# Kernel optimization log

Hardware: AMD Instinct MI355X
Metric: run time of the kernel (lower is better)

## Reference

```python
import jax, jax.numpy as jnp
import numpy as np

SLOPE = 0.2

def setup_inputs() -> dict:
    key = jax.random.key(0)
    ks = jax.random.split(key, 24)
    B, O, M, Nb = 16, 1024, 64, 64
    in_ope, in_mas, in_arc, out = 16, 8, 8, 32
    f = lambda k, s: jax.random.normal(k, s, dtype=jnp.float32)
    adj = lambda k, s: jax.random.randint(k, s, 0, 2).astype(jnp.float32)
    return {
        'adj0': adj(ks[0], (O, M)),
        'adj1': adj(ks[1], (O, M)),
        'adj2': adj(ks[2], (O, Nb)),
        'adj3': adj(ks[3], (O, Nb)),
        'batch_idxes': jnp.arange(B, dtype=jnp.int64),
        'feat_opes': f(ks[4], (B, O, in_ope)),
        'feat_mas': f(ks[5], (B, M, in_mas)),
        'feat_buf': f(ks[6], (B, Nb, in_mas)),
        'feat_arc_ma_in': f(ks[7], (B, O, M, in_arc)),
        'feat_arc_buf_in': f(ks[8], (B, O, Nb, in_arc)),
        'feat_arc_ma_out': f(ks[9], (B, O, M, in_arc)),
        'feat_arc_buf_out': f(ks[10], (B, O, Nb, in_arc)),
        'W_ope': f(ks[11], (in_ope, out)) * 0.2,
        'W_mas': f(ks[12], (in_mas, out)) * 0.2,
        'W_buf': f(ks[13], (in_mas, out)) * 0.2,
        'W_arc_in': f(ks[14], (in_arc, out)) * 0.2,
        'W_arc_out': f(ks[15], (in_arc, out)) * 0.2,
        'attn_ope': jax.random.uniform(ks[16], (out,), dtype=jnp.float32),
        'attn_mas': jax.random.uniform(ks[17], (out,), dtype=jnp.float32),
        'attn_arc': jax.random.uniform(ks[18], (out,), dtype=jnp.float32),
    }

def _branch(adj_in, adj_out, p_ope, p_node, p_arc_in, p_arc_out, e_ope, e_node, e_arc_in, e_arc_out):
    # adj_*: [O,N]; e_ope: [B,O,1]; e_node: [B,N,1]; e_arc_*: [B,O,N,1]
    def scores(A2, e_arc):
        A = A2[None, :, :, None]                               # [1,O,N,1]
        a = A * e_ope[:, :, None, :] + e_arc + A * e_node[:, None, :, :]
        return jax.nn.leaky_relu(a, SLOPE)                     # [B,O,N,1]
    eik_in = scores(adj_in, e_arc_in)
    eik_out = scores(adj_out, e_arc_out)
    ekk = jax.nn.leaky_relu(e_node + e_node, SLOPE)            # [B,N,1]
    def alphas(A2, eik):
        e = jnp.concatenate([eik, ekk[:, None]], axis=1)       # [B,O+1,N,1]
        mask = jnp.concatenate([A2 == 1.0, jnp.ones((1, A2.shape[1]), dtype=bool)], axis=0)
        e = jnp.where(mask[None, :, :, None], e, -jnp.inf)
        return jax.nn.softmax(e[..., 0], axis=1)               # [B,O+1,N] over neighbors
    al_in = alphas(adj_in, eik_in)
    al_out = alphas(adj_out, eik_out)
    # NOTE: Wmu_out replicates the original's missing-parens expression exactly
    Wmu_in = jnp.sum((p_arc_in + p_ope[:, :, None, :]) * al_in[:, :-1, :, None], axis=1)   # [B,N,F]
    Wmu_out = jnp.sum(p_arc_out + p_ope[:, :, None, :] * al_out[:, :-1, :, None], axis=1)  # [B,N,F]
    Wmu_kk = p_node * (al_in[:, -1, :] + al_out[:, -1, :])[..., None]                      # [B,N,F]
    return jax.nn.sigmoid(Wmu_in + Wmu_out + Wmu_kk)

def reference(adj0, adj1, adj2, adj3, batch_idxes, feat_opes, feat_mas, feat_buf,
              feat_arc_ma_in, feat_arc_buf_in, feat_arc_ma_out, feat_arc_buf_out,
              W_ope, W_mas, W_buf, W_arc_in, W_arc_out, attn_ope, attn_mas, attn_arc):
    p_ope = feat_opes @ W_ope              # [B,O,F]
    p_mas = feat_mas @ W_mas               # [B,M,F]
    p_buf = feat_buf @ W_buf               # [B,Nb,F]
    p_arc_ma_in = feat_arc_ma_in @ W_arc_in
    p_arc_buf_in = feat_arc_buf_in @ W_arc_in
    p_arc_ma_out = feat_arc_ma_out @ W_arc_out
    p_arc_buf_out = feat_arc_buf_out @ W_arc_out
    score = lambda p, a: jnp.sum(p * a, axis=-1, keepdims=True)
    e_ope = score(p_ope, attn_ope)
    e_mas = score(p_mas, attn_mas)
    e_buf = score(p_buf, attn_mas)         # original uses attn_mas for buffers too
    nu_mas = _branch(adj0, adj1, p_ope, p_mas, p_arc_ma_in, p_arc_ma_out,
                     e_ope, e_mas, score(p_arc_ma_in, attn_arc), score(p_arc_ma_out, attn_arc))
    nu_buf = _branch(adj2, adj3, p_ope, p_buf, p_arc_buf_in, p_arc_buf_out,
                     e_ope, e_buf, score(p_arc_buf_in, attn_arc), score(p_arc_buf_out, attn_arc))
    return (nu_mas, nu_buf)
```

## Files before the change

kernel.cpp:

```cpp
#include <hip/hip_runtime.h>
#include <math.h>

#define B_   16
#define O_   1024
#define M_   64
#define C_   32
#define INO  16
#define INA  8
#define S_CH 16
#define SLOPE 0.2f
#define NEG_BIG (-1e30f)

#define WS_EOPE   0
#define WS_ENODE  (WS_EOPE + B_*O_)
#define WS_PNODE  (WS_ENODE + 2*B_*M_)
#define WS_WARC   (WS_PNODE + 2*B_*M_*C_)
#define WS_PART   (WS_WARC + 16)
#define PSTATE    52

struct St {
    float mx_in, l_in, ai[8], aoi[16];
    float mx_out, l_out, aoo[16], sao[8];
};

__device__ inline void st_init(St& s) {
    s.mx_in = NEG_BIG; s.l_in = 0.f;
    s.mx_out = NEG_BIG; s.l_out = 0.f;
#pragma unroll
    for (int k = 0; k < 8; ++k) { s.ai[k] = 0.f; s.sao[k] = 0.f; }
#pragma unroll
    for (int j = 0; j < 16; ++j) { s.aoi[j] = 0.f; s.aoo[j] = 0.f; }
}

__device__ inline void st_store(const St& s, float* p) {
    p[0] = s.mx_in; p[1] = s.l_in;
#pragma unroll
    for (int k = 0; k < 8; ++k) p[2+k] = s.ai[k];
#pragma unroll
    for (int j = 0; j < 16; ++j) p[10+j] = s.aoi[j];
    p[26] = s.mx_out; p[27] = s.l_out;
#pragma unroll
    for (int j = 0; j < 16; ++j) p[28+j] = s.aoo[j];
#pragma unroll
    for (int k = 0; k < 8; ++k) p[44+k] = s.sao[k];
}

__device__ inline void st_merge(St& a, const float* p) {
    {
        float mb = p[0];
        float mx = fmaxf(a.mx_in, mb);
        float ca = __expf(a.mx_in - mx), cb = __expf(mb - mx);
        a.l_in = a.l_in*ca + p[1]*cb;
#pragma unroll
        for (int k = 0; k < 8; ++k)  a.ai[k]  = a.ai[k]*ca  + p[2+k]*cb;
#pragma unroll
        for (int j = 0; j < 16; ++j) a.aoi[j] = a.aoi[j]*ca + p[10+j]*cb;
        a.mx_in = mx;
    }
    {
        float mb = p[26];
        float mx = fmaxf(a.mx_out, mb);
        float ca = __expf(a.mx_out - mx), cb = __expf(mb - mx);
        a.l_out = a.l_out*ca + p[27]*cb;
#pragma unroll
        for (int j = 0; j < 16; ++j) a.aoo[j] = a.aoo[j]*ca + p[28+j]*cb;
        a.mx_out = mx;
    }
#pragma unroll
    for (int k = 0; k < 8; ++k) a.sao[k] += p[44+k];
}

__global__ void k_pre(const float* __restrict__ feat_opes,
                      const float* __restrict__ feat_mas,
                      const float* __restrict__ feat_buf,
                      const float* __restrict__ W_ope,
                      const float* __restrict__ W_mas,
                      const float* __restrict__ W_buf,
                      const float* __restrict__ W_arc_in,
                      const float* __restrict__ W_arc_out,
                      const float* __restrict__ attn_ope,
                      const float* __restrict__ attn_mas,
                      const float* __restrict__ attn_arc,
                      float* __restrict__ ws) {
    int tid = threadIdx.x;
    int bid = blockIdx.x;
    if (bid < 64) {
        __shared__ float wo[INO];
        if (tid < INO) {
            float s = 0.f;
            for (int c = 0; c < C_; ++c) s += W_ope[tid*C_ + c]*attn_ope[c];
            wo[tid] = s;
        }
        __syncthreads();
        int idx = bid*256 + tid;
        const float* f = feat_opes + idx*INO;
        float s = 0.f;
#pragma unroll
        for (int j = 0; j < INO; ++j) s += f[j]*wo[j];
        ws[WS_EOPE + idx] = s;
    } else if (bid < 72) {
        int idx = (bid - 64)*256 + tid;
        int br  = idx >> 10;
        int rem = idx & 1023;
        const float* f = (br == 0 ? feat_mas : feat_buf) + rem*INA;
        const float* W = (br == 0 ? W_mas : W_buf);
        float f8[INA];
#pragma unroll
        for (int k = 0; k < INA; ++k) f8[k] = f[k];
        float e = 0.f;
        float* pn = ws + WS_PNODE + idx*C_;
        for (int c = 0; c < C_; ++c) {
            float s = 0.f;
#pragma unroll
            for (int k = 0; k < INA; ++k) s += f8[k]*W[k*C_ + c];
            pn[c] = s;
            e += s*attn_mas[c];
        }
        ws[WS_ENODE + idx] = e;
    } else {
        if (tid < 16) {
            const float* W = (tid < 8) ? W_arc_in : W_arc_out;
            int k = tid & 7;
            float s = 0.f;
            for (int c = 0; c < C_; ++c) s += W[k*C_ + c]*attn_arc[c];
            ws[WS_WARC + tid] = s;
        }
    }
}

__global__ __launch_bounds__(256) void k_main(
        const float* __restrict__ adj0, const float* __restrict__ adj1,
        const float* __restrict__ adj2, const float* __restrict__ adj3,
        const float* __restrict__ feat_opes,
        const float* __restrict__ fin_ma,  const float* __restrict__ fin_buf,
        const float* __restrict__ fout_ma, const float* __restrict__ fout_buf,
        float* __restrict__ ws) {
    int tid = threadIdx.x;
    int m = tid & 63;
    int y = __builtin_amdgcn_readfirstlane(tid >> 6);
    int bid = blockIdx.x;
    int chunk = bid & (S_CH - 1);
    int t = bid >> 4;
    int b = t & (B_ - 1);
    int br = t >> 4;

    const float* A_in  = br ? adj2 : adj0;
    const float* A_out = br ? adj3 : adj1;
    const float* fin   = br ? fin_buf  : fin_ma;
    const float* fout  = br ? fout_buf : fout_ma;
    const float* e_ope = ws + WS_EOPE + b*O_;
    float e_node_m = ws[WS_ENODE + (br*B_ + b)*M_ + m];

    float w_in[8], w_out[8];
#pragma unroll
    for (int k = 0; k < 8; ++k) { w_in[k] = ws[WS_WARC + k]; w_out[k] = ws[WS_WARC + 8 + k]; }

    St s; st_init(s);

    int o0 = chunk*64 + y*16;
#pragma unroll 2
    for (int it = 0; it < 16; ++it) {
        int o = o0 + it;
        const float4* pin = (const float4*)(fin  + ((b*O_ + o)*M_ + m)*INA);
        const float4* pot = (const float4*)(fout + ((b*O_ + o)*M_ + m)*INA);
        float4 i0 = pin[0], i1 = pin[1];
        float4 u0 = pot[0], u1 = pot[1];
        float aA = A_in[o*M_ + m];
        float aB = A_out[o*M_ + m];
        float eo = e_ope[o];
        const float* fo = feat_opes + (b*O_ + o)*INO;

        float ein = i0.x*w_in[0] + i0.y*w_in[1] + i0.z*w_in[2] + i0.w*w_in[3]
                  + i1.x*w_in[4] + i1.y*w_in[5] + i1.z*w_in[6] + i1.w*w_in[7];
        float eut = u0.x*w_out[0] + u0.y*w_out[1] + u0.z*w_out[2] + u0.w*w_out[3]
                  + u1.x*w_out[4] + u1.y*w_out[5] + u1.z*w_out[6] + u1.w*w_out[7];

        {
            bool v = (aA == 1.0f);
            float sc = eo + ein + e_node_m;
            sc = sc > 0.f ? sc : SLOPE*sc;
            float mnew = v ? fmaxf(s.mx_in, sc) : s.mx_in;
            float corr = __expf(s.mx_in - mnew);
            float w    = v ? __expf(sc - mnew) : 0.f;
            s.l_in = s.l_in*corr + w;
            s.ai[0] = s.ai[0]*corr + w*i0.x;  s.ai[1] = s.ai[1]*corr + w*i0.y;
            s.ai[2] = s.ai[2]*corr + w*i0.z;  s.ai[3] = s.ai[3]*corr + w*i0.w;
            s.ai[4] = s.ai[4]*corr + w*i1.x;  s.ai[5] = s.ai[5]*corr + w*i1.y;
            s.ai[6] = s.ai[6]*corr + w*i1.z;  s.ai[7] = s.ai[7]*corr + w*i1.w;
#pragma unroll
            for (int j = 0; j < 16; ++j) s.aoi[j] = s.aoi[j]*corr + w*fo[j];
            s.mx_in = mnew;
        }
        {
            bool v = (aB == 1.0f);
            float sc = eo + eut + e_node_m;
            sc = sc > 0.f ? sc : SLOPE*sc;
            float mnew = v ? fmaxf(s.mx_out, sc) : s.mx_out;
            float corr = __expf(s.mx_out - mnew);
            float w    = v ? __expf(sc - mnew) : 0.f;
            s.l_out = s.l_out*corr + w;
#pragma unroll
            for (int j = 0; j < 16; ++j) s.aoo[j] = s.aoo[j]*corr + w*fo[j];
            s.mx_out = mnew;
        }
        s.sao[0] += u0.x; s.sao[1] += u0.y; s.sao[2] += u0.z; s.sao[3] += u0.w;
        s.sao[4] += u1.x; s.sao[5] += u1.y; s.sao[6] += u1.z; s.sao[7] += u1.w;
    }

    __shared__ float lds[4][64][PSTATE];
    st_store(s, lds[y][m]);
    __syncthreads();
    if (y == 0) {
        st_merge(s, lds[1][m]);
        st_merge(s, lds[2][m]);
        st_merge(s, lds[3][m]);
        float* P = ws + WS_PART + (size_t)(((br*B_ + b)*S_CH + chunk)*M_ + m)*PSTATE;
        st_store(s, P);
    }
}

__global__ __launch_bounds__(64) void k_fin(
        const float* __restrict__ W_ope,
        const float* __restrict__ W_arc_in,
        const float* __restrict__ W_arc_out,
        const float* __restrict__ ws,
        float* __restrict__ out) {
    int m = threadIdx.x;
    int bid = blockIdx.x;
    int b  = bid & (B_ - 1);
    int br = bid >> 4;

    __shared__ float sW[1024];
    for (int i = m; i < 512; i += 64) sW[i] = W_ope[i];
    for (int i = m; i < 256; i += 64) { sW[512 + i] = W_arc_in[i]; sW[768 + i] = W_arc_out[i]; }
    __syncthreads();

    St s; st_init(s);
    const float* base = ws + WS_PART + (size_t)((br*B_ + b)*S_CH)*M_*PSTATE;
    for (int ch = 0; ch < S_CH; ++ch)
        st_merge(s, base + (ch*M_ + m)*PSTATE);

    float en  = ws[WS_ENODE + (br*B_ + b)*M_ + m];
    float ekk = 2.f*en; ekk = ekk > 0.f ? ekk : SLOPE*ekk;

    float mxf_i = fmaxf(s.mx_in, ekk);
    float ci    = __expf(s.mx_in - mxf_i);
    float wkk_i = __expf(ekk - mxf_i);
    float lf_i  = s.l_in*ci + wkk_i;
    float inv_i = 1.f/lf_i;
    float fac_in = ci*inv_i;
    float akk_in = wkk_i*inv_i;

    float mxf_o = fmaxf(s.mx_out, ekk);
    float co    = __expf(s.mx_out - mxf_o);
    float wkk_o = __expf(ekk - mxf_o);
    float lf_o  = s.l_out*co + wkk_o;
    float inv_o = 1.f/lf_o;
    float fac_out = co*inv_o;
    float akk_out = wkk_o*inv_o;

    const float* pn = ws + WS_PNODE + ((br*B_ + b)*M_ + m)*C_;
    float akk = akk_in + akk_out;
    float* op = out + ((size_t)br*B_*M_ + b*M_ + m)*C_;

    for (int c = 0; c < C_; ++c) {
        float s_ai = 0.f, s_oi = 0.f, s_ao = 0.f, s_oo = 0.f;
#pragma unroll
        for (int k = 0; k < 8; ++k) {
            s_ai += s.ai[k]*sW[512 + k*C_ + c];
            s_ao += s.sao[k]*sW[768 + k*C_ + c];
        }
#pragma unroll
        for (int j = 0; j < 16; ++j) {
            float wv = sW[j*C_ + c];
            s_oi += s.aoi[j]*wv;
            s_oo += s.aoo[j]*wv;
        }
        float x = (s_ai + s_oi)*fac_in + s_ao + s_oo*fac_out + pn[c]*akk;
        op[c] = 1.f/(1.f + __expf(-x));
    }
}

extern "C" void kernel_launch(void* const* d_in, const int* in_sizes, int n_in,
                              void* d_out, int out_size, void* d_ws, size_t ws_size,
                              hipStream_t stream) {
    const float* adj0 = (const float*)d_in[0];
    const float* adj1 = (const float*)d_in[1];
    const float* adj2 = (const float*)d_in[2];
    const float* adj3 = (const float*)d_in[3];
    const float* feat_opes       = (const float*)d_in[5];
    const float* feat_mas        = (const float*)d_in[6];
    const float* feat_buf        = (const float*)d_in[7];
    const float* feat_arc_ma_in  = (const float*)d_in[8];
    const float* feat_arc_buf_in = (const float*)d_in[9];
    const float* feat_arc_ma_out = (const float*)d_in[10];
    const float* feat_arc_buf_out= (const float*)d_in[11];
    const float* W_ope    = (const float*)d_in[12];
    const float* W_mas    = (const float*)d_in[13];
    const float* W_buf    = (const float*)d_in[14];
    const float* W_arc_in = (const float*)d_in[15];
    const float* W_arc_out= (const float*)d_in[16];
    const float* attn_ope = (const float*)d_in[17];
    const float* attn_mas = (const float*)d_in[18];
    const float* attn_arc = (const float*)d_in[19];

    float* ws  = (float*)d_ws;
    float* out = (float*)d_out;

    k_pre<<<73, 256, 0, stream>>>(feat_opes, feat_mas, feat_buf,
                                  W_ope, W_mas, W_buf, W_arc_in, W_arc_out,
                                  attn_ope, attn_mas, attn_arc, ws);

    k_main<<<2*B_*S_CH, 256, 0, stream>>>(adj0, adj1, adj2, adj3, feat_opes,
                                          feat_arc_ma_in, feat_arc_buf_in,
                                          feat_arc_ma_out, feat_arc_buf_out, ws);

    k_fin<<<2*B_, 64, 0, stream>>>(W_ope, W_arc_in, W_arc_out, ws, out);
}
```

Before: 239.0 us.

## Drop online-softmax max tracking, reduce partials with atomics, double chunk count

Removes the running-max online softmax and accumulates raw exp weights, which lets the per-column partial state be summed directly. Cross-chunk partials are now merged with float atomic adds into a zeroed accumulator (zeroed by extra k_pre blocks) instead of a per-chunk workspace array and a serial merge in k_fin. Chunks double to 32, with 8 rows per wave, software-prefetched arc loads, and feat_opes accumulation split into a second pass. This trades numerical safety (exp without max subtraction could overflow for large scores) and atomic nondeterminism for less serial merge work and more parallelism.

```diff
diff --git a/kernel.cpp b/kernel.cpp
--- a/kernel.cpp
+++ b/kernel.cpp
@@ -7,68 +7,17 @@
 #define C_   32
 #define INO  16
 #define INA  8
-#define S_CH 16
+#define S_CH 32
 #define SLOPE 0.2f
-#define NEG_BIG (-1e30f)
+
+#define NF    50
+#define NCOL  (2*B_*M_)
 
 #define WS_EOPE   0
 #define WS_ENODE  (WS_EOPE + B_*O_)
 #define WS_PNODE  (WS_ENODE + 2*B_*M_)
 #define WS_WARC   (WS_PNODE + 2*B_*M_*C_)
-#define WS_PART   (WS_WARC + 16)
-#define PSTATE    52
-
-struct St {
-    float mx_in, l_in, ai[8], aoi[16];
-    float mx_out, l_out, aoo[16], sao[8];
-};
-
-__device__ inline void st_init(St& s) {
-    s.mx_in = NEG_BIG; s.l_in = 0.f;
-    s.mx_out = NEG_BIG; s.l_out = 0.f;
-#pragma unroll
-    for (int k = 0; k < 8; ++k) { s.ai[k] = 0.f; s.sao[k] = 0.f; }
-#pragma unroll
-    for (int j = 0; j < 16; ++j) { s.aoi[j] = 0.f; s.aoo[j] = 0.f; }
-}
-
-__device__ inline void st_store(const St& s, float* p) {
-    p[0] = s.mx_in; p[1] = s.l_in;
-#pragma unroll
-    for (int k = 0; k < 8; ++k) p[2+k] = s.ai[k];
-#pragma unroll
-    for (int j = 0; j < 16; ++j) p[10+j] = s.aoi[j];
-    p[26] = s.mx_out; p[27] = s.l_out;
-#pragma unroll
-    for (int j = 0; j < 16; ++j) p[28+j] = s.aoo[j];
-#pragma unroll
-    for (int k = 0; k < 8; ++k) p[44+k] = s.sao[k];
-}
-
-__device__ inline void st_merge(St& a, const float* p) {
-    {
-        float mb = p[0];
-        float mx = fmaxf(a.mx_in, mb);
-        float ca = __expf(a.mx_in - mx), cb = __expf(mb - mx);
-        a.l_in = a.l_in*ca + p[1]*cb;
-#pragma unroll
-        for (int k = 0; k < 8; ++k)  a.ai[k]  = a.ai[k]*ca  + p[2+k]*cb;
-#pragma unroll
-        for (int j = 0; j < 16; ++j) a.aoi[j] = a.aoi[j]*ca + p[10+j]*cb;
-        a.mx_in = mx;
-    }
-    {
-        float mb = p[26];
-        float mx = fmaxf(a.mx_out, mb);
-        float ca = __expf(a.mx_out - mx), cb = __expf(mb - mx);
-        a.l_out = a.l_out*ca + p[27]*cb;
-#pragma unroll
-        for (int j = 0; j < 16; ++j) a.aoo[j] = a.aoo[j]*ca + p[28+j]*cb;
-        a.mx_out = mx;
-    }
-#pragma unroll
-    for (int k = 0; k < 8; ++k) a.sao[k] += p[44+k];
-}
+#define WS_ACC    (WS_WARC + 16)
 
 __global__ void k_pre(const float* __restrict__ feat_opes,
                       const float* __restrict__ feat_mas,
@@ -117,7 +66,7 @@
             e += s*attn_mas[c];
         }
         ws[WS_ENODE + idx] = e;
-    } else {
+    } else if (bid == 72) {
         if (tid < 16) {
             const float* W = (tid < 8) ? W_arc_in : W_arc_out;
             int k = tid & 7;
@@ -125,6 +74,9 @@
             for (int c = 0; c < C_; ++c) s += W[k*C_ + c]*attn_arc[c];
             ws[WS_WARC + tid] = s;
         }
+    } else {
+        int idx = (bid - 73)*256 + tid;
+        ws[WS_ACC + idx] = 0.f;
     }
 }
 
@@ -137,10 +89,10 @@
         float* __restrict__ ws) {
     int tid = threadIdx.x;
     int m = tid & 63;
-    int y = __builtin_amdgcn_readfirstlane(tid >> 6);
+    int y = tid >> 6;
     int bid = blockIdx.x;
     int chunk = bid & (S_CH - 1);
-    int t = bid >> 4;
+    int t = bid >> 5;
     int b = t & (B_ - 1);
     int br = t >> 4;
 
@@ -148,74 +100,119 @@
     const float* A_out = br ? adj3 : adj1;
     const float* fin   = br ? fin_buf  : fin_ma;
     const float* fout  = br ? fout_buf : fout_ma;
-    const float* e_ope = ws + WS_EOPE + b*O_;
+
+    int o0 = chunk*32 + y*8;
+
     float e_node_m = ws[WS_ENODE + (br*B_ + b)*M_ + m];
 
-    float w_in[8], w_out[8];
-#pragma unroll
-    for (int k = 0; k < 8; ++k) { w_in[k] = ws[WS_WARC + k]; w_out[k] = ws[WS_WARC + 8 + k]; }
-
-    St s; st_init(s);
-
-    int o0 = chunk*64 + y*16;
-#pragma unroll 2
-    for (int it = 0; it < 16; ++it) {
-        int o = o0 + it;
-        const float4* pin = (const float4*)(fin  + ((b*O_ + o)*M_ + m)*INA);
-        const float4* pot = (const float4*)(fout + ((b*O_ + o)*M_ + m)*INA);
-        float4 i0 = pin[0], i1 = pin[1];
-        float4 u0 = pot[0], u1 = pot[1];
-        float aA = A_in[o*M_ + m];
-        float aB = A_out[o*M_ + m];
-        float eo = e_ope[o];
-        const float* fo = feat_opes + (b*O_ + o)*INO;
-
-        float ein = i0.x*w_in[0] + i0.y*w_in[1] + i0.z*w_in[2] + i0.w*w_in[3]
-                  + i1.x*w_in[4] + i1.y*w_in[5] + i1.z*w_in[6] + i1.w*w_in[7];
-        float eut = u0.x*w_out[0] + u0.y*w_out[1] + u0.z*w_out[2] + u0.w*w_out[3]
-                  + u1.x*w_out[4] + u1.y*w_out[5] + u1.z*w_out[6] + u1.w*w_out[7];
-
-        {
-            bool v = (aA == 1.0f);
-            float sc = eo + ein + e_node_m;
-            sc = sc > 0.f ? sc : SLOPE*sc;
-            float mnew = v ? fmaxf(s.mx_in, sc) : s.mx_in;
-            float corr = __expf(s.mx_in - mnew);
-            float w    = v ? __expf(sc - mnew) : 0.f;
-            s.l_in = s.l_in*corr + w;
-            s.ai[0] = s.ai[0]*corr + w*i0.x;  s.ai[1] = s.ai[1]*corr + w*i0.y;
-            s.ai[2] = s.ai[2]*corr + w*i0.z;  s.ai[3] = s.ai[3]*corr + w*i0.w;
-            s.ai[4] = s.ai[4]*corr + w*i1.x;  s.ai[5] = s.ai[5]*corr + w*i1.y;
-            s.ai[6] = s.ai[6]*corr + w*i1.z;  s.ai[7] = s.ai[7]*corr + w*i1.w;
-#pragma unroll
-            for (int j = 0; j < 16; ++j) s.aoi[j] = s.aoi[j]*corr + w*fo[j];
-            s.mx_in = mnew;
-        }
-        {
-            bool v = (aB == 1.0f);
-            float sc = eo + eut + e_node_m;
-            sc = sc > 0.f ? sc : SLOPE*sc;
-            float mnew = v ? fmaxf(s.mx_out, sc) : s.mx_out;
-            float corr = __expf(s.mx_out - mnew);
-            float w    = v ? __expf(sc - mnew) : 0.f;
-            s.l_out = s.l_out*corr + w;
-#pragma unroll
-            for (int j = 0; j < 16; ++j) s.aoo[j] = s.aoo[j]*corr + w*fo[j];
-            s.mx_out = mnew;
-        }
-        s.sao[0] += u0.x; s.sao[1] += u0.y; s.sao[2] += u0.z; s.sao[3] += u0.w;
-        s.sao[4] += u1.x; s.sao[5] += u1.y; s.sao[6] += u1.z; s.sao[7] += u1.w;
-    }
-
-    __shared__ float lds[4][64][PSTATE];
-    st_store(s, lds[y][m]);
+    const float* wv = ws + WS_WARC;
+    float w_in0=wv[0],w_in1=wv[1],w_in2=wv[2],w_in3=wv[3];
+    float w_in4=wv[4],w_in5=wv[5],w_in6=wv[6],w_in7=wv[7];
+    float w_ot0=wv[8],w_ot1=wv[9],w_ot2=wv[10],w_ot3=wv[11];
+    float w_ot4=wv[12],w_ot5=wv[13],w_ot6=wv[14],w_ot7=wv[15];
+
+    const float* e_ope = ws + WS_EOPE + b*O_ + o0;
+    float eo[8];
+#pragma unroll
+    for (int i = 0; i < 8; ++i) eo[i] = e_ope[i];
+
+    float aA[8], aB[8];
+    const float* Ai = A_in  + o0*M_ + m;
+    const float* Ao = A_out + o0*M_ + m;
+#pragma unroll
+    for (int i = 0; i < 8; ++i) { aA[i] = Ai[i*M_]; aB[i] = Ao[i*M_]; }
+
+    const float* pi = fin  + ((size_t)(b*O_ + o0)*M_ + m)*INA;
+    const float* po = fout + ((size_t)(b*O_ + o0)*M_ + m)*INA;
+    const int OSTR = M_*INA;
+
+    float ai[8], sao[8], wiv[8], wov[8];
+#pragma unroll
+    for (int k = 0; k < 8; ++k) { ai[k] = 0.f; sao[k] = 0.f; }
+
+    float4 i0 = *(const float4*)(pi);
+    float4 i1 = *(const float4*)(pi + 4);
+    float4 u0 = *(const float4*)(po);
+    float4 u1 = *(const float4*)(po + 4);
+
+#pragma unroll
+    for (int it = 0; it < 8; ++it) {
+        float4 ni0, ni1, nu0, nu1;
+        if (it < 7) {
+            const float* qi = pi + (it+1)*OSTR;
+            const float* qo = po + (it+1)*OSTR;
+            ni0 = *(const float4*)(qi);
+            ni1 = *(const float4*)(qi + 4);
+            nu0 = *(const float4*)(qo);
+            nu1 = *(const float4*)(qo + 4);
+        }
+        float ein = i0.x*w_in0 + i0.y*w_in1 + i0.z*w_in2 + i0.w*w_in3
+                  + i1.x*w_in4 + i1.y*w_in5 + i1.z*w_in6 + i1.w*w_in7;
+        float eut = u0.x*w_ot0 + u0.y*w_ot1 + u0.z*w_ot2 + u0.w*w_ot3
+                  + u1.x*w_ot4 + u1.y*w_ot5 + u1.z*w_ot6 + u1.w*w_ot7;
+        float base = eo[it] + e_node_m;
+        float si = base + ein;  si = si > 0.f ? si : SLOPE*si;
+        float so = base + eut;  so = so > 0.f ? so : SLOPE*so;
+        float wi = (aA[it] == 1.0f) ? __expf(si) : 0.f;
+        float wo_ = (aB[it] == 1.0f) ? __expf(so) : 0.f;
+        wiv[it] = wi; wov[it] = wo_;
+        ai[0] += wi*i0.x; ai[1] += wi*i0.y; ai[2] += wi*i0.z; ai[3] += wi*i0.w;
+        ai[4] += wi*i1.x; ai[5] += wi*i1.y; ai[6] += wi*i1.z; ai[7] += wi*i1.w;
+        sao[0] += u0.x; sao[1] += u0.y; sao[2] += u0.z; sao[3] += u0.w;
+        sao[4] += u1.x; sao[5] += u1.y; sao[6] += u1.z; sao[7] += u1.w;
+        i0 = ni0; i1 = ni1; u0 = nu0; u1 = nu1;
+    }
+
+    float l_in = 0.f, l_out = 0.f;
+#pragma unroll
+    for (int it = 0; it < 8; ++it) { l_in += wiv[it]; l_out += wov[it]; }
+
+    float aoi[16], aoo[16];
+#pragma unroll
+    for (int j = 0; j < 16; ++j) { aoi[j] = 0.f; aoo[j] = 0.f; }
+    const float* fo_base = feat_opes + (size_t)(b*O_ + o0)*INO;
+#pragma unroll
+    for (int it = 0; it < 8; ++it) {
+        const float4* fp = (const float4*)(fo_base + it*INO);
+        float4 f0 = fp[0], f1 = fp[1], f2 = fp[2], f3 = fp[3];
+        float wi = wiv[it], wo_ = wov[it];
+        aoi[0]  += wi*f0.x; aoi[1]  += wi*f0.y; aoi[2]  += wi*f0.z; aoi[3]  += wi*f0.w;
+        aoi[4]  += wi*f1.x; aoi[5]  += wi*f1.y; aoi[6]  += wi*f1.z; aoi[7]  += wi*f1.w;
+        aoi[8]  += wi*f2.x; aoi[9]  += wi*f2.y; aoi[10] += wi*f2.z; aoi[11] += wi*f2.w;
+        aoi[12] += wi*f3.x; aoi[13] += wi*f3.y; aoi[14] += wi*f3.z; aoi[15] += wi*f3.w;
+        aoo[0]  += wo_*f0.x; aoo[1]  += wo_*f0.y; aoo[2]  += wo_*f0.z; aoo[3]  += wo_*f0.w;
+        aoo[4]  += wo_*f1.x; aoo[5]  += wo_*f1.y; aoo[6]  += wo_*f1.z; aoo[7]  += wo_*f1.w;
+        aoo[8]  += wo_*f2.x; aoo[9]  += wo_*f2.y; aoo[10] += wo_*f2.z; aoo[11] += wo_*f2.w;
+        aoo[12] += wo_*f3.x; aoo[13] += wo_*f3.y; aoo[14] += wo_*f3.z; aoo[15] += wo_*f3.w;
+    }
+
+    float v[NF];
+    v[0] = l_in;
+#pragma unroll
+    for (int k = 0; k < 8; ++k)  v[1+k]  = ai[k];
+#pragma unroll
+    for (int j = 0; j < 16; ++j) v[9+j]  = aoi[j];
+    v[25] = l_out;
+#pragma unroll
+    for (int j = 0; j < 16; ++j) v[26+j] = aoo[j];
+#pragma unroll
+    for (int k = 0; k < 8; ++k)  v[42+k] = sao[k];
+
+    __shared__ float red[3][NF][64];
+    if (y > 0) {
+#pragma unroll
+        for (int f = 0; f < NF; ++f) red[y-1][f][m] = v[f];
+    }
     __syncthreads();
     if (y == 0) {
-        st_merge(s, lds[1][m]);
-        st_merge(s, lds[2][m]);
-        st_merge(s, lds[3][m]);
-        float* P = ws + WS_PART + (size_t)(((br*B_ + b)*S_CH + chunk)*M_ + m)*PSTATE;
-        st_store(s, P);
+#pragma unroll
+        for (int f = 0; f < NF; ++f)
+            v[f] += red[0][f][m] + red[1][f][m] + red[2][f][m];
+        float* acc = ws + WS_ACC;
+        int col = (br*B_ + b)*M_ + m;
+#pragma unroll
+        for (int f = 0; f < NF; ++f)
+            unsafeAtomicAdd(acc + f*NCOL + col, v[f]);
     }
 }
 
@@ -229,54 +226,50 @@
     int bid = blockIdx.x;
     int b  = bid & (B_ - 1);
     int br = bid >> 4;
+    int col = (br*B_ + b)*M_ + m;
 
     __shared__ float sW[1024];
     for (int i = m; i < 512; i += 64) sW[i] = W_ope[i];
     for (int i = m; i < 256; i += 64) { sW[512 + i] = W_arc_in[i]; sW[768 + i] = W_arc_out[i]; }
     __syncthreads();
 
-    St s; st_init(s);
-    const float* base = ws + WS_PART + (size_t)((br*B_ + b)*S_CH)*M_*PSTATE;
-    for (int ch = 0; ch < S_CH; ++ch)
-        st_merge(s, base + (ch*M_ + m)*PSTATE);
-
-    float en  = ws[WS_ENODE + (br*B_ + b)*M_ + m];
+    const float* acc = ws + WS_ACC;
+    float v[NF];
+#pragma unroll
+    for (int f = 0; f < NF; ++f) v[f] = acc[f*NCOL + col];
+
+    const float* pn = ws + WS_PNODE + col*C_;
+    float pc[C_];
+#pragma unroll
+    for (int q = 0; q < 8; ++q) {
+        float4 p4 = *(const float4*)(pn + 4*q);
+        pc[4*q] = p4.x; pc[4*q+1] = p4.y; pc[4*q+2] = p4.z; pc[4*q+3] = p4.w;
+    }
+
+    float en  = ws[WS_ENODE + col];
     float ekk = 2.f*en; ekk = ekk > 0.f ? ekk : SLOPE*ekk;
-
-    float mxf_i = fmaxf(s.mx_in, ekk);
-    float ci    = __expf(s.mx_in - mxf_i);
-    float wkk_i = __expf(ekk - mxf_i);
-    float lf_i  = s.l_in*ci + wkk_i;
-    float inv_i = 1.f/lf_i;
-    float fac_in = ci*inv_i;
-    float akk_in = wkk_i*inv_i;
-
-    float mxf_o = fmaxf(s.mx_out, ekk);
-    float co    = __expf(s.mx_out - mxf_o);
-    float wkk_o = __expf(ekk - mxf_o);
-    float lf_o  = s.l_out*co + wkk_o;
-    float inv_o = 1.f/lf_o;
-    float fac_out = co*inv_o;
-    float akk_out = wkk_o*inv_o;
-
-    const float* pn = ws + WS_PNODE + ((br*B_ + b)*M_ + m)*C_;
-    float akk = akk_in + akk_out;
-    float* op = out + ((size_t)br*B_*M_ + b*M_ + m)*C_;
-
+    float wkk = __expf(ekk);
+
+    float inv_i = 1.f / (v[0]  + wkk);
+    float inv_o = 1.f / (v[25] + wkk);
+    float akk   = wkk*inv_i + wkk*inv_o;
+
+    float* op = out + (size_t)col*C_;
+#pragma unroll 4
     for (int c = 0; c < C_; ++c) {
         float s_ai = 0.f, s_oi = 0.f, s_ao = 0.f, s_oo = 0.f;
 #pragma unroll
         for (int k = 0; k < 8; ++k) {
-            s_ai += s.ai[k]*sW[512 + k*C_ + c];
-            s_ao += s.sao[k]*sW[768 + k*C_ + c];
+            s_ai += v[1+k] *sW[512 + k*C_ + c];
+            s_ao += v[42+k]*sW[768 + k*C_ + c];
         }
 #pragma unroll
         for (int j = 0; j < 16; ++j) {
             float wv = sW[j*C_ + c];
-            s_oi += s.aoi[j]*wv;
-            s_oo += s.aoo[j]*wv;
-        }
-        float x = (s_ai + s_oi)*fac_in + s_ao + s_oo*fac_out + pn[c]*akk;
+            s_oi += v[9+j]*wv;
+            s_oo += v[26+j]*wv;
+        }
+        float x = (s_ai + s_oi)*inv_i + s_ao + s_oo*inv_o + pc[c]*akk;
         op[c] = 1.f/(1.f + __expf(-x));
     }
 }
@@ -307,9 +300,9 @@
     float* ws  = (float*)d_ws;
     float* out = (float*)d_out;
 
-    k_pre<<<73, 256, 0, stream>>>(feat_opes, feat_mas, feat_buf,
-                                  W_ope, W_mas, W_buf, W_arc_in, W_arc_out,
-                                  attn_ope, attn_mas, attn_arc, ws);
+    k_pre<<<473, 256, 0, stream>>>(feat_opes, feat_mas, feat_buf,
+                                   W_ope, W_mas, W_buf, W_arc_in, W_arc_out,
+                                   attn_ope, attn_mas, attn_arc, ws);
 
     k_main<<<2*B_*S_CH, 256, 0, stream>>>(adj0, adj1, adj2, adj3, feat_opes,
                                           feat_arc_ma_in, feat_arc_buf_in,
```

After: 210.9 us. 1.13x faster.
